# Optimization experiments

Hardware: AMD Instinct MI355X
Metric: run time of the kernel (lower is better)

Reference implementation:

```python
import jax, jax.numpy as jnp
from jax import lax
import numpy as np

B, N, CF = 16, 4096, 64
NPOINT, NSAMPLE = 1024, 32
MLP = (64, 64, 128)
IN_CH = CF + 3
EPS = 1e-5


def _fps(xyz, npoint):
    # Farthest point sampling; deterministic start at index 0 (original uses a random start).
    Bn = xyz.shape[0]
    d0 = jnp.full(xyz.shape[:2], 1e10, xyz.dtype)
    f0 = jnp.zeros((Bn,), jnp.int32)
    def step(carry, _):
        dist, far = carry
        c = jnp.take_along_axis(xyz, far[:, None, None], axis=1)  # (B,1,3)
        d = jnp.sum((xyz - c) ** 2, axis=-1)                      # (B,N)
        dist = jnp.minimum(dist, d)
        return (dist, jnp.argmax(dist, axis=1).astype(jnp.int32)), far
    _, idxs = lax.scan(step, (d0, f0), None, length=npoint)
    return jnp.transpose(idxs)  # (B, npoint)


def _gather(pts, idx):
    # pts (B,N,C), idx (B,...) int -> (B,...,C)
    return jax.vmap(lambda p, i: p[i])(pts, idx)


def _bn_relu(x, g, b, axes):
    # training-mode batch norm (batch statistics), channel axis = 1
    m = jnp.mean(x, axes, keepdims=True)
    v = jnp.var(x, axes, keepdims=True)
    sh = (1, -1) + (1,) * (x.ndim - 2)
    return jax.nn.relu((x - m) * lax.rsqrt(v + EPS) * g.reshape(sh) + b.reshape(sh))


def _forward(xyz, points, density, params):
    fps_idx = _fps(xyz, NPOINT)
    new_xyz = _gather(xyz, fps_idx)  # (B,S,3)
    # source query_ball_point sorts distances and keeps the nsample nearest -> kNN
    d = (jnp.sum(new_xyz ** 2, -1)[:, :, None] + jnp.sum(xyz ** 2, -1)[:, None, :]
         - 2.0 * jnp.einsum('bsc,bnc->bsn', new_xyz, xyz))  # (B,S,N)
    _, idx = lax.top_k(-d, NSAMPLE)  # (B,S,ns) nearest neighbors
    gxyz = _gather(xyz, idx) - new_xyz[:, :, None, :]           # (B,S,ns,3)
    gpts = _gather(jnp.transpose(points, (0, 2, 1)), idx)       # (B,S,ns,CF)
    x = jnp.transpose(jnp.concatenate([gxyz, gpts], -1), (0, 3, 1, 2))  # (B,IN_CH,S,ns)
    (w0, b0, g0, be0, w1, b1, g1, be1, w2, b2, g2, be2, wd, bd, gd, bed) = params
    for w, b, g, be in ((w0, b0, g0, be0), (w1, b1, g1, be1), (w2, b2, g2, be2)):
        x = _bn_relu(jnp.einsum('oc,bcsk->bosk', w, x) + b[None, :, None, None], g, be, (0, 2, 3))
    # density weighting at sampled centers
    dcen = jnp.transpose(_gather(jnp.transpose(density, (0, 2, 1)), fps_idx), (0, 2, 1))  # (B,1,S)
    dw = _bn_relu(jnp.einsum('oc,bcs->bos', wd, dcen) + bd[None, :, None], gd, bed, (0, 2))  # (B,Cout,S)
    x = x * dw[..., None]
    return new_xyz, jnp.max(x, axis=-1)  # (B,S,3), (B,Cout,S)


def setup_inputs() -> dict:
    key = jax.random.key(0)
    ks = jax.random.split(key, 3)
    inp = {
        'xyz': jax.random.normal(ks[0], (B, N, 3), jnp.float32),
        'points': jax.random.normal(ks[1], (B, CF, N), jnp.float32),
        'density': jax.random.uniform(ks[2], (B, 1, N), jnp.float32),
    }
    chans = (IN_CH,) + MLP
    for i in range(3):
        cin, cout = chans[i], chans[i + 1]
        inp[f'w{i}'] = jax.random.normal(jax.random.fold_in(key, 10 + i), (cout, cin), jnp.float32) / np.sqrt(cin).astype(np.float32)
        inp[f'b{i}'] = jnp.zeros((cout,), jnp.float32)
        inp[f'g{i}'] = jnp.ones((cout,), jnp.float32)
        inp[f'be{i}'] = jnp.zeros((cout,), jnp.float32)
    inp['wd'] = jax.random.normal(jax.random.fold_in(key, 20), (MLP[-1], 1), jnp.float32)
    inp['bd'] = jnp.zeros((MLP[-1],), jnp.float32)
    inp['gd'] = jnp.ones((MLP[-1],), jnp.float32)
    inp['bed'] = jnp.zeros((MLP[-1],), jnp.float32)
    return inp


def reference(xyz, points, density, w0, b0, g0, be0, w1, b1, g1, be1, w2, b2, g2, be2, wd, bd, gd, bed):
    return _forward(xyz, points, density,
                    (w0, b0, g0, be0, w1, b1, g1, be1, w2, b2, g2, be2, wd, bd, gd, bed))
```

## Files before the change

### kernel.cpp

```cpp
#include <hip/hip_runtime.h>
#include <hip/hip_bf16.h>
#include <stdint.h>

#define NB 16
#define NN 4096
#define NCF 64
#define NS 1024
#define NK 32
#define NPTS (NB*NS*NK)
#define CIN 67
#define EPSV 1e-5f

static __device__ __forceinline__ float fmul(float a, float b){ return __fmul_rn(a,b); }
static __device__ __forceinline__ float fadd(float a, float b){ return __fadd_rn(a,b); }
static __device__ __forceinline__ float fsub(float a, float b){ return __fsub_rn(a,b); }

typedef float f2 __attribute__((ext_vector_type(2)));
#define PK_ADD(d,a,b) asm("v_pk_add_f32 %0, %1, %2" : "=v"(d) : "v"(a), "v"(b))
#define PK_MUL(d,a,b) asm("v_pk_mul_f32 %0, %1, %2" : "=v"(d) : "v"(a), "v"(b))

static __device__ __forceinline__ unsigned short f2b(float f){
  unsigned u = __float_as_uint(f);
  return (unsigned short)((u + 0x7FFFu + ((u>>16)&1u)) >> 16);
}

template<int CTRL>
static __device__ __forceinline__ float dppmax_f32(float x){
  float o = __uint_as_float((unsigned)__builtin_amdgcn_update_dpp(
      0, (int)__float_as_uint(x), CTRL, 0xf, 0xf, true));
  return fmaxf(x, o);
}
static __device__ __forceinline__ float wave_max63_f32(float x){
  x = dppmax_f32<0x111>(x);
  x = dppmax_f32<0x112>(x);
  x = dppmax_f32<0x114>(x);
  x = dppmax_f32<0x118>(x);
  x = dppmax_f32<0x142>(x);
  x = dppmax_f32<0x143>(x);
  return x;
}
template<int CTRL>
static __device__ __forceinline__ float dppadd_f32(float x){
  float o = __uint_as_float((unsigned)__builtin_amdgcn_update_dpp(
      0, (int)__float_as_uint(x), CTRL, 0xf, 0xf, true));
  return x + o;
}
static __device__ __forceinline__ float wave_sum63_f32(float x){
  x = dppadd_f32<0x111>(x);
  x = dppadd_f32<0x112>(x);
  x = dppadd_f32<0x114>(x);
  x = dppadd_f32<0x118>(x);
  x = dppadd_f32<0x142>(x);
  x = dppadd_f32<0x143>(x);
  return x;
}
static __device__ __forceinline__ float half_sum31_f32(float x){
  x = dppadd_f32<0x111>(x);
  x = dppadd_f32<0x112>(x);
  x = dppadd_f32<0x114>(x);
  x = dppadd_f32<0x118>(x);
  x = dppadd_f32<0x142>(x);
  return x;
}
static __device__ __forceinline__ float group8_max_f32(float x){
  x = dppmax_f32<0xB1>(x);
  x = dppmax_f32<0x4E>(x);
  x = dppmax_f32<0x141>(x);
  return x;
}
static __device__ __forceinline__ unsigned long long readlane_u64(unsigned long long v, int l){
  unsigned lo = (unsigned)__builtin_amdgcn_readlane((int)(unsigned)v, l);
  unsigned hi = (unsigned)__builtin_amdgcn_readlane((int)(unsigned)(v>>32), l);
  return ((unsigned long long)hi<<32) | lo;
}
static __device__ __forceinline__ unsigned long long wave_shr1_u64(unsigned long long x){
  unsigned lo = (unsigned)__builtin_amdgcn_update_dpp(
      0, (int)(unsigned)x, 0x138, 0xf, 0xf, true);
  unsigned hi = (unsigned)__builtin_amdgcn_update_dpp(
      0, (int)(unsigned)(x>>32), 0x138, 0xf, 0xf, true);
  return ((unsigned long long)hi<<32) | lo;
}

__global__ __launch_bounds__(256) void prep_kernel(const float* __restrict__ pts,
    const float* __restrict__ xyz, float* __restrict__ ptsT, float* __restrict__ sqx){
  int blk = blockIdx.x;
  int b = blk >> 4;
  int n = ((blk & 15) << 8) + threadIdx.x;
  const float* src = pts + (size_t)b*NCF*NN + n;
  float v[NCF];
  #pragma unroll
  for (int c=0;c<NCF;c++) v[c] = src[(size_t)c*NN];
  float4* dst = (float4*)(ptsT + ((size_t)b*NN + n)*NCF);
  #pragma unroll
  for (int j=0;j<16;j++) dst[j] = make_float4(v[4*j],v[4*j+1],v[4*j+2],v[4*j+3]);
  const float* xp = xyz + ((size_t)b*NN + n)*3;
  float x=xp[0], y=xp[1], z=xp[2];
  sqx[(size_t)b*NN+n] = fadd(fadd(fmul(x,x),fmul(y,y)),fmul(z,z));
}

#define FT 256
__global__ __launch_bounds__(FT) void fps_kernel(const float* __restrict__ xyz,
    int* __restrict__ fidx, float* __restrict__ newxyz){
  int b = blockIdx.x;
  __shared__ float4 s4[NN];
  __shared__ unsigned long long candK[2][4];
  __shared__ float4 candC[2][4];
  const int tid = threadIdx.x;
  const int lane = tid & 63;
  const int wv = tid >> 6;
  for (int i = tid; i < NN; i += FT){
    const float* p = xyz + ((size_t)b*NN + i)*3;
    s4[i] = make_float4(p[0], p[1], p[2], 0.f);
  }
  __syncthreads();
  f2 px[8], py[8], pz[8], d2[8];
  #pragma unroll
  for (int m=0;m<8;m++){
    float4 a = s4[tid*16 + 2*m];
    float4 c = s4[tid*16 + 2*m + 1];
    px[m] = (f2){a.x, c.x};
    py[m] = (f2){a.y, c.y};
    pz[m] = (f2){a.z, c.z};
    d2[m] = (f2){1e10f, 1e10f};
  }
  int far = 0;
  float4 cc = s4[0];
  for (int s=0;s<NS;s++){
    if (tid==0){
      fidx[b*NS+s] = far;
      float* o = newxyz + ((size_t)b*NS+s)*3;
      o[0]=cc.x; o[1]=cc.y; o[2]=cc.z;
    }
    f2 ncx = (f2){-cc.x,-cc.x}, ncy = (f2){-cc.y,-cc.y}, ncz = (f2){-cc.z,-cc.z};
    float bv = -1.0f; int bj = 0;
    #pragma unroll
    for (int m=0;m<8;m++){
      f2 dx,dy,dz,xx,yy,zz,ss,dd;
      PK_ADD(dx, px[m], ncx);
      PK_ADD(dy, py[m], ncy);
      PK_ADD(dz, pz[m], ncz);
      PK_MUL(xx, dx, dx);
      PK_MUL(yy, dy, dy);
      PK_ADD(ss, xx, yy);
      PK_MUL(zz, dz, dz);
      PK_ADD(dd, ss, zz);
      float u0 = fminf(d2[m].x, dd.x);
      float u1 = fminf(d2[m].y, dd.y);
      d2[m].x = u0; d2[m].y = u1;
      if (u0 > bv){ bv = u0; bj = 2*m; }
      if (u1 > bv){ bv = u1; bj = 2*m+1; }
    }
    int nbest = (tid<<4) + bj;
    float mv = wave_max63_f32(bv);
    float mvu = __uint_as_float((unsigned)__builtin_amdgcn_readlane(
        (int)__float_as_uint(mv), 63));
    unsigned long long tiedm = __ballot(bv == mvu);
    int wl = __ffsll(tiedm) - 1;
    unsigned nwin = (unsigned)__builtin_amdgcn_readlane(nbest, wl);
    if (lane == wl){
      float4 cw = s4[nwin];
      candK[s&1][wv] = ((unsigned long long)__float_as_uint(mvu) << 32)
                     | (unsigned long long)(unsigned)~nwin;
      candC[s&1][wv] = cw;
    }
    __syncthreads();
    const ulonglong2* kp = (const ulonglong2*)candK[s&1];
    ulonglong2 k01v = kp[0], k23v = kp[1];
    float4 C0 = candC[s&1][0], C1 = candC[s&1][1];
    float4 C2 = candC[s&1][2], C3 = candC[s&1][3];
    bool a01 = k01v.y > k01v.x;
    unsigned long long k01 = a01 ? k01v.y : k01v.x;
    float4 c01; c01.x = a01?C1.x:C0.x; c01.y = a01?C1.y:C0.y; c01.z = a01?C1.z:C0.z;
    bool a23 = k23v.y > k23v.x;
    unsigned long long k23 = a23 ? k23v.y : k23v.x;
    float4 c23; c23.x = a23?C3.x:C2.x; c23.y = a23?C3.y:C2.y; c23.z = a23?C3.z:C2.z;
    bool af = k23 > k01;
    unsigned long long kk = af ? k23 : k01;
    cc.x = af?c23.x:c01.x; cc.y = af?c23.y:c01.y; cc.z = af?c23.z:c01.z;
    far = (int)(~(unsigned)kk) & (NN-1);
  }
}

__global__ __launch_bounds__(256) void dcen_kernel(const float* __restrict__ density,
    const int* __restrict__ fidx, float* __restrict__ dcen){
  int i = blockIdx.x*256 + threadIdx.x;
  int b = i >> 10;
  dcen[i] = density[(size_t)b*NN + fidx[i]];
}

__global__ __launch_bounds__(256) void dstats_kernel(const float* __restrict__ dcen,
    float* __restrict__ dstat){
  float s=0.f, q=0.f;
  for (int i=threadIdx.x; i<NB*NS; i+=256){ float v=dcen[i]; s+=v; q+=v*v; }
  __shared__ float ls[256], lq[256];
  ls[threadIdx.x]=s; lq[threadIdx.x]=q;
  __syncthreads();
  for (int off=128; off>0; off>>=1){
    if (threadIdx.x<off){ ls[threadIdx.x]+=ls[threadIdx.x+off]; lq[threadIdx.x]+=lq[threadIdx.x+off]; }
    __syncthreads();
  }
  if (threadIdx.x==0){
    float m = ls[0]/(float)(NB*NS);
    dstat[0]=m; dstat[1]=lq[0]/(float)(NB*NS) - m*m;
  }
}

__global__ __launch_bounds__(256) void knn_kernel(const float* __restrict__ xyz,
    const float* __restrict__ sqx, const float* __restrict__ newxyz,
    int* __restrict__ kidx){
  const int lane = threadIdx.x & 63;
  const int g = blockIdx.x*4 + (threadIdx.x >> 6);
  const int b = g >> 10;
  const float* cp = newxyz + (size_t)g*3;
  const float cx=cp[0], cy=cp[1], cz=cp[2];
  const float sqc = fadd(fadd(fmul(cx,cx),fmul(cy,cy)),fmul(cz,cz));
  const float* xb  = xyz + (size_t)b*NN*3;
  const float* sqb = sqx + (size_t)b*NN;
  unsigned long long kept  = ~0ULL;
  unsigned long long worst = ~0ULL;
  for (int n0=0; n0<NN; n0+=64){
    const int n = n0 + lane;
    const float* xp = xb + (size_t)n*3;
    float x=xp[0], y=xp[1], z=xp[2];
    float dot = fadd(fadd(fmul(cx,x),fmul(cy,y)),fmul(cz,z));
    float d = fsub(fadd(sqc, sqb[n]), fmul(2.0f,dot));
    unsigned u = __float_as_uint(d);
    u = (u & 0x80000000u) ? ~u : (u | 0x80000000u);
    unsigned long long ck = ((unsigned long long)u << 32) | (unsigned)n;
    unsigned long long mask = __ballot(ck < worst);
    while (mask){
      const int l = __ffsll(mask) - 1;
      mask &= mask - 1;
      const unsigned long long k = readlane_u64(ck, l);
      if (k < worst){
        bool m = kept > k;
        unsigned long long M = __ballot(m) << 1;
        unsigned long long sh = wave_shr1_u64(kept);
        bool msh = (M >> lane) & 1ULL;
        unsigned long long ins = msh ? sh : k;
        kept = m ? ins : kept;
        worst = readlane_u64(kept, 31);
      }
    }
  }
  if (lane < 32) kidx[(size_t)g*NK + lane] = (int)(kept & 0xFFFFFFFFULL);
}

__global__ __launch_bounds__(256) void conv1_kernel(const float* __restrict__ xyz,
    const float* __restrict__ ptsT, const float* __restrict__ newxyz,
    const int* __restrict__ kidx, const float* __restrict__ w0,
    const float* __restrict__ b0, unsigned short* __restrict__ z1,
    float* __restrict__ partial){
  __shared__ float si[CIN][128];
  __shared__ float sw[CIN][64];
  __shared__ float sbias[64];
  const int tid = threadIdx.x;
  for (int i = tid; i < CIN*64; i += 256){
    int o = i / CIN, c = i - o*CIN;
    sw[c][o] = w0[i];
  }
  if (tid < 64) sbias[tid] = b0[tid];
  const int p0 = blockIdx.x * 128;
  if (tid < 128){
    const int p = p0 + tid;
    const int g = p >> 5;
    const int b = g >> 10;
    const int n = kidx[p];
    const float* xp = xyz + ((size_t)b*NN + n)*3;
    const float* cp = newxyz + (size_t)g*3;
    si[0][tid] = xp[0]-cp[0];
    si[1][tid] = xp[1]-cp[1];
    si[2][tid] = xp[2]-cp[2];
    const float4* pr = (const float4*)(ptsT + ((size_t)b*NN + n)*NCF);
    #pragma unroll
    for (int j=0;j<16;j++){
      float4 v = pr[j];
      si[3+4*j][tid]=v.x; si[4+4*j][tid]=v.y; si[5+4*j][tid]=v.z; si[6+4*j][tid]=v.w;
    }
  }
  __syncthreads();
  const int og = tid >> 6;
  const int pg = tid & 63;
  float acc0[16], acc1[16];
  #pragma unroll
  for (int j=0;j<16;j++){ float bv = sbias[og*16+j]; acc0[j]=bv; acc1[j]=bv; }
  for (int c=0;c<CIN;c++){
    float2 a = *(const float2*)&si[c][2*pg];
    const float4* wr = (const float4*)&sw[c][og*16];
    #pragma unroll
    for (int q=0;q<4;q++){
      float4 w = wr[q];
      acc0[4*q+0]+=a.x*w.x; acc0[4*q+1]+=a.x*w.y; acc0[4*q+2]+=a.x*w.z; acc0[4*q+3]+=a.x*w.w;
      acc1[4*q+0]+=a.y*w.x; acc1[4*q+1]+=a.y*w.y; acc1[4*q+2]+=a.y*w.z; acc1[4*q+3]+=a.y*w.w;
    }
  }
  unsigned v[8];
  #pragma unroll
  for (int j=0;j<8;j++) v[j] = (unsigned)f2b(acc0[2*j]) | ((unsigned)f2b(acc0[2*j+1])<<16);
  uint4* d0 = (uint4*)(z1 + (size_t)(p0+2*pg)*64 + og*16);
  d0[0]=make_uint4(v[0],v[1],v[2],v[3]); d0[1]=make_uint4(v[4],v[5],v[6],v[7]);
  #pragma unroll
  for (int j=0;j<8;j++) v[j] = (unsigned)f2b(acc1[2*j]) | ((unsigned)f2b(acc1[2*j+1])<<16);
  uint4* d1 = (uint4*)(z1 + (size_t)(p0+2*pg+1)*64 + og*16);
  d1[0]=make_uint4(v[0],v[1],v[2],v[3]); d1[1]=make_uint4(v[4],v[5],v[6],v[7]);
  #pragma unroll
  for (int j=0;j<16;j++){
    float s = wave_sum63_f32(acc0[j]+acc1[j]);
    float q = wave_sum63_f32(acc0[j]*acc0[j] + acc1[j]*acc1[j]);
    if (pg==63){
      partial[(size_t)blockIdx.x*128 + og*16 + j] = s;
      partial[(size_t)blockIdx.x*128 + 64 + og*16 + j] = q;
    }
  }
}

__global__ __launch_bounds__(256) void conv2_kernel(const unsigned short* __restrict__ z1,
    const float* __restrict__ w1, const float* __restrict__ b1,
    const float* __restrict__ scale1, const float* __restrict__ shift1,
    unsigned short* __restrict__ z2, float* __restrict__ partial){
  __shared__ float si[64][128];
  __shared__ float sw[64][64];
  __shared__ float sbias[64];
  const int tid = threadIdx.x;
  for (int i = tid; i < 64*64; i += 256){
    int o = i >> 6, c = i & 63;
    sw[c][o] = w1[i];
  }
  if (tid < 64) sbias[tid] = b1[tid];
  const int p0 = blockIdx.x * 128;
  if (tid < 128){
    const uint4* zr = (const uint4*)(z1 + (size_t)(p0 + tid)*64);
    #pragma unroll
    for (int j=0;j<8;j++){
      uint4 vv = zr[j];
      unsigned a[4] = {vv.x, vv.y, vv.z, vv.w};
      #pragma unroll
      for (int t=0;t<4;t++){
        int c = j*8 + t*2;
        float lo = __uint_as_float(a[t] << 16);
        float hi = __uint_as_float(a[t] & 0xFFFF0000u);
        si[c][tid]   = fmaxf(lo*scale1[c]   + shift1[c],   0.0f);
        si[c+1][tid] = fmaxf(hi*scale1[c+1] + shift1[c+1], 0.0f);
      }
    }
  }
  __syncthreads();
  const int og = tid >> 6;
  const int pg = tid & 63;
  float acc0[16], acc1[16];
  #pragma unroll
  for (int j=0;j<16;j++){ float bv = sbias[og*16+j]; acc0[j]=bv; acc1[j]=bv; }
  for (int c=0;c<64;c++){
    float2 a = *(const float2*)&si[c][2*pg];
    const float4* wr = (const float4*)&sw[c][og*16];
    #pragma unroll
    for (int q=0;q<4;q++){
      float4 w = wr[q];
      acc0[4*q+0]+=a.x*w.x; acc0[4*q+1]+=a.x*w.y; acc0[4*q+2]+=a.x*w.z; acc0[4*q+3]+=a.x*w.w;
      acc1[4*q+0]+=a.y*w.x; acc1[4*q+1]+=a.y*w.y; acc1[4*q+2]+=a.y*w.z; acc1[4*q+3]+=a.y*w.w;
    }
  }
  unsigned v[8];
  #pragma unroll
  for (int j=0;j<8;j++) v[j] = (unsigned)f2b(acc0[2*j]) | ((unsigned)f2b(acc0[2*j+1])<<16);
  uint4* d0 = (uint4*)(z2 + (size_t)(p0+2*pg)*64 + og*16);
  d0[0]=make_uint4(v[0],v[1],v[2],v[3]); d0[1]=make_uint4(v[4],v[5],v[6],v[7]);
  #pragma unroll
  for (int j=0;j<8;j++) v[j] = (unsigned)f2b(acc1[2*j]) | ((unsigned)f2b(acc1[2*j+1])<<16);
  uint4* d1 = (uint4*)(z2 + (size_t)(p0+2*pg+1)*64 + og*16);
  d1[0]=make_uint4(v[0],v[1],v[2],v[3]); d1[1]=make_uint4(v[4],v[5],v[6],v[7]);
  #pragma unroll
  for (int j=0;j<16;j++){
    float s = wave_sum63_f32(acc0[j]+acc1[j]);
    float q = wave_sum63_f32(acc0[j]*acc0[j] + acc1[j]*acc1[j]);
    if (pg==63){
      partial[(size_t)blockIdx.x*128 + og*16 + j] = s;
      partial[(size_t)blockIdx.x*128 + 64 + og*16 + j] = q;
    }
  }
}

__global__ __launch_bounds__(256) void conv3_kernel(const unsigned short* __restrict__ z2,
    const float* __restrict__ w2, const float* __restrict__ b2,
    const float* __restrict__ scale2, const float* __restrict__ shift2,
    float* __restrict__ m3, float* __restrict__ partial){
  __shared__ float si[64][128];
  __shared__ float sw[64][128];
  const int tid = threadIdx.x;
  for (int i = tid; i < 64*128; i += 256){
    int o = i >> 6, c = i & 63;
    sw[c][o] = w2[i];
  }
  const int p0 = blockIdx.x * 128;
  if (tid < 128){
    const uint4* zr = (const uint4*)(z2 + (size_t)(p0 + tid)*64);
    #pragma unroll
    for (int j=0;j<8;j++){
      uint4 vv = zr[j];
      unsigned a[4]={vv.x,vv.y,vv.z,vv.w};
      #pragma unroll
      for (int t=0;t<4;t++){
        int c = j*8+t*2;
        float lo=__uint_as_float(a[t]<<16), hi=__uint_as_float(a[t]&0xFFFF0000u);
        si[c][tid]   = fmaxf(lo*scale2[c]+shift2[c],0.f);
        si[c+1][tid] = fmaxf(hi*scale2[c+1]+shift2[c+1],0.f);
      }
    }
  }
  __syncthreads();
  const int og = tid >> 5;
  const int pg = tid & 31;
  float acc[4][16];
  const float4* bq = (const float4*)(b2 + og*16);
  #pragma unroll
  for (int q=0;q<4;q++){
    float4 bb = bq[q];
    #pragma unroll
    for (int p=0;p<4;p++){ acc[p][4*q]=bb.x; acc[p][4*q+1]=bb.y; acc[p][4*q+2]=bb.z; acc[p][4*q+3]=bb.w; }
  }
  for (int c=0;c<64;c++){
    float4 a = *(const float4*)&si[c][pg*4];
    const float4* wr = (const float4*)&sw[c][og*16];
    float ap[4] = {a.x, a.y, a.z, a.w};
    #pragma unroll
    for (int q=0;q<4;q++){
      float4 w = wr[q];
      #pragma unroll
      for (int p=0;p<4;p++){
        acc[p][4*q+0]+=ap[p]*w.x; acc[p][4*q+1]+=ap[p]*w.y;
        acc[p][4*q+2]+=ap[p]*w.z; acc[p][4*q+3]+=ap[p]*w.w;
      }
    }
  }
  float mx[16];
  #pragma unroll
  for (int j=0;j<16;j++){
    float m = fmaxf(fmaxf(acc[0][j],acc[1][j]), fmaxf(acc[2][j],acc[3][j]));
    mx[j] = group8_max_f32(m);
  }
  if ((pg & 7)==0){
    const int center = blockIdx.x*4 + (pg>>3);
    float4* mp = (float4*)(m3 + (size_t)center*128 + og*16);
    #pragma unroll
    for (int q=0;q<4;q++) mp[q] = make_float4(mx[4*q],mx[4*q+1],mx[4*q+2],mx[4*q+3]);
  }
  #pragma unroll
  for (int j=0;j<16;j++){
    float s = half_sum31_f32(acc[0][j]+acc[1][j]+acc[2][j]+acc[3][j]);
    float q = half_sum31_f32(acc[0][j]*acc[0][j]+acc[1][j]*acc[1][j]
                            +acc[2][j]*acc[2][j]+acc[3][j]*acc[3][j]);
    if (pg==31){
      partial[(size_t)blockIdx.x*256 + og*16 + j] = s;
      partial[(size_t)blockIdx.x*256 + 128 + og*16 + j] = q;
    }
  }
}

__global__ __launch_bounds__(256) void mkbn_kernel(const float* __restrict__ partial,
    int nrows, int stride, const float* __restrict__ g, const float* __restrict__ be,
    float* __restrict__ scale, float* __restrict__ shift, float inv_count){
  const int c = blockIdx.x;
  const int C = gridDim.x;
  float s=0.f, q=0.f;
  for (int r=threadIdx.x; r<nrows; r+=256){
    s += partial[(size_t)r*stride + c];
    q += partial[(size_t)r*stride + C + c];
  }
  __shared__ float ls[256], lq[256];
  ls[threadIdx.x]=s; lq[threadIdx.x]=q;
  __syncthreads();
  for (int off=128; off>0; off>>=1){
    if (threadIdx.x < off){ ls[threadIdx.x]+=ls[threadIdx.x+off]; lq[threadIdx.x]+=lq[threadIdx.x+off]; }
    __syncthreads();
  }
  if (threadIdx.x==0){
    float mean = ls[0]*inv_count;
    float var  = lq[0]*inv_count - mean*mean;
    float sc = g[c]*rsqrtf(var + EPSV);
    scale[c]=sc; shift[c]=be[c]-mean*sc;
  }
}

__global__ __launch_bounds__(256) void final_kernel(const float* __restrict__ m3,
    const float* __restrict__ dcen, const float* __restrict__ scale3,
    const float* __restrict__ shift3, const float* __restrict__ wd,
    const float* __restrict__ bd, const float* __restrict__ gd,
    const float* __restrict__ bed, const float* __restrict__ dstat,
    float* __restrict__ out){
  size_t i = (size_t)blockIdx.x*256 + threadIdx.x;
  int s  = (int)(i & 1023);
  int ch = (int)((i >> 10) & 127);
  int b  = (int)(i >> 17);
  float mean_d = dstat[0], var_d = dstat[1];
  float w = wd[ch];
  float meanp = w*mean_d + bd[ch];
  float varp  = w*w*var_d;
  float dsc = gd[ch]*rsqrtf(varp + EPSV);
  float dsh = bed[ch] - meanp*dsc;
  float pre = w*dcen[b*NS+s] + bd[ch];
  float dw  = fmaxf(dsc*pre + dsh, 0.0f);
  float z   = m3[((size_t)(b*NS+s))*128 + ch];
  float x   = fmaxf(scale3[ch]*z + shift3[ch], 0.0f);
  out[i] = x*dw;
}

extern "C" void kernel_launch(void* const* d_in, const int* in_sizes, int n_in,
                              void* d_out, int out_size, void* d_ws, size_t ws_size,
                              hipStream_t stream){
  const float* xyz     = (const float*)d_in[0];
  const float* points  = (const float*)d_in[1];
  const float* density = (const float*)d_in[2];
  const float* w0 = (const float*)d_in[3];
  const float* b0 = (const float*)d_in[4];
  const float* g0 = (const float*)d_in[5];
  const float* be0= (const float*)d_in[6];
  const float* w1 = (const float*)d_in[7];
  const float* b1 = (const float*)d_in[8];
  const float* g1 = (const float*)d_in[9];
  const float* be1= (const float*)d_in[10];
  const float* w2 = (const float*)d_in[11];
  const float* b2 = (const float*)d_in[12];
  const float* g2 = (const float*)d_in[13];
  const float* be2= (const float*)d_in[14];
  const float* wd = (const float*)d_in[15];
  const float* bd = (const float*)d_in[16];
  const float* gd = (const float*)d_in[17];
  const float* bed= (const float*)d_in[18];

  float* out = (float*)d_out;
  float* newxyz = out;
  float* out1   = out + (size_t)NB*NS*3;

  float* ptsT = (float*)d_ws;
  float* sqx  = ptsT + (size_t)NB*NN*NCF;
  int*   fidx = (int*)(sqx + (size_t)NB*NN);
  float* dcen = (float*)(fidx + NB*NS);
  int*   kidx = (int*)(dcen + NB*NS);
  unsigned short* z1 = (unsigned short*)(kidx + NPTS);
  unsigned short* z2 = z1 + (size_t)NPTS*64;
  float* m3   = (float*)(z2 + (size_t)NPTS*64);
  float* p1   = m3 + (size_t)NB*NS*128;
  float* p2   = p1 + 4096*128;
  float* p3   = p2 + 4096*128;
  float* bnp  = p3 + 4096*256;
  float* dstat= bnp + 512;

  hipLaunchKernelGGL(prep_kernel,  dim3(256),  dim3(256), 0, stream, points, xyz, ptsT, sqx);
  hipLaunchKernelGGL(fps_kernel,   dim3(NB),   dim3(FT),  0, stream, xyz, fidx, newxyz);
  hipLaunchKernelGGL(dcen_kernel,  dim3(64),   dim3(256), 0, stream, density, fidx, dcen);
  hipLaunchKernelGGL(dstats_kernel,dim3(1),    dim3(256), 0, stream, dcen, dstat);
  hipLaunchKernelGGL(knn_kernel,   dim3(4096), dim3(256), 0, stream, xyz, sqx, newxyz, kidx);
  hipLaunchKernelGGL(conv1_kernel, dim3(4096), dim3(256), 0, stream, xyz, ptsT, newxyz, kidx, w0, b0, z1, p1);
  hipLaunchKernelGGL(mkbn_kernel,  dim3(64),   dim3(256), 0, stream, p1, 4096, 128, g0, be0, bnp+0,   bnp+64,  1.0f/(float)NPTS);
  hipLaunchKernelGGL(conv2_kernel, dim3(4096), dim3(256), 0, stream, z1, w1, b1, bnp+0, bnp+64, z2, p2);
  hipLaunchKernelGGL(mkbn_kernel,  dim3(64),   dim3(256), 0, stream, p2, 4096, 128, g1, be1, bnp+128, bnp+192, 1.0f/(float)NPTS);
  hipLaunchKernelGGL(conv3_kernel, dim3(4096), dim3(256), 0, stream, z2, w2, b2, bnp+128, bnp+192, m3, p3);
  hipLaunchKernelGGL(mkbn_kernel,  dim3(128),  dim3(256), 0, stream, p3, 4096, 256, g2, be2, bnp+256, bnp+384, 1.0f/(float)NPTS);
  hipLaunchKernelGGL(final_kernel, dim3(8192), dim3(256), 0, stream, m3, dcen, bnp+256, bnp+384, wd, bd, gd, bed, dstat, out1);
}
```

Before: 1.331 ms.

## Widen FPS to 512 threads and use packed FP32 FMA in conv kernels

The FPS kernel now runs 512 threads per batch with 8 points per thread. The cross-wave reduction is simplified: each wave publishes only its packed distance/index key, and the winner's coordinates are read from shared memory after the max. The conv1, conv2 and conv3 inner loops switch from scalar FMAs to v_pk_fma_f32 on float2 accumulators, and the batch-norm statistic reductions are packed the same way. This aims to cut per-iteration FPS latency and halve FMA issue count in the convolutions, at the cost of an extra dependent LDS read per FPS step and more inline-asm register pressure.

```diff
diff --git a/kernel.cpp b/kernel.cpp
--- a/kernel.cpp
+++ b/kernel.cpp
@@ -18,10 +18,18 @@
 typedef float f2 __attribute__((ext_vector_type(2)));
 #define PK_ADD(d,a,b) asm("v_pk_add_f32 %0, %1, %2" : "=v"(d) : "v"(a), "v"(b))
 #define PK_MUL(d,a,b) asm("v_pk_mul_f32 %0, %1, %2" : "=v"(d) : "v"(a), "v"(b))
+#define PK_FMA(d,a,b) asm("v_pk_fma_f32 %0, %1, %2, %0" : "+v"(d) : "v"(a), "v"(b))
+static __device__ __forceinline__ f2 pk_add(f2 a, f2 b){ f2 d; PK_ADD(d,a,b); return d; }
+static __device__ __forceinline__ f2 pk_mul(f2 a, f2 b){ f2 d; PK_MUL(d,a,b); return d; }
 
 static __device__ __forceinline__ unsigned short f2b(float f){
   unsigned u = __float_as_uint(f);
   return (unsigned short)((u + 0x7FFFu + ((u>>16)&1u)) >> 16);
+}
+
+static __device__ __forceinline__ unsigned long long umax64(unsigned long long a,
+                                                            unsigned long long b){
+  return a > b ? a : b;
 }
 
 template<int CTRL>
@@ -39,33 +47,36 @@
   x = dppmax_f32<0x143>(x);
   return x;
 }
-template<int CTRL>
-static __device__ __forceinline__ float dppadd_f32(float x){
-  float o = __uint_as_float((unsigned)__builtin_amdgcn_update_dpp(
-      0, (int)__float_as_uint(x), CTRL, 0xf, 0xf, true));
-  return x + o;
-}
-static __device__ __forceinline__ float wave_sum63_f32(float x){
-  x = dppadd_f32<0x111>(x);
-  x = dppadd_f32<0x112>(x);
-  x = dppadd_f32<0x114>(x);
-  x = dppadd_f32<0x118>(x);
-  x = dppadd_f32<0x142>(x);
-  x = dppadd_f32<0x143>(x);
-  return x;
-}
-static __device__ __forceinline__ float half_sum31_f32(float x){
-  x = dppadd_f32<0x111>(x);
-  x = dppadd_f32<0x112>(x);
-  x = dppadd_f32<0x114>(x);
-  x = dppadd_f32<0x118>(x);
-  x = dppadd_f32<0x142>(x);
-  return x;
-}
 static __device__ __forceinline__ float group8_max_f32(float x){
   x = dppmax_f32<0xB1>(x);
   x = dppmax_f32<0x4E>(x);
   x = dppmax_f32<0x141>(x);
+  return x;
+}
+template<int CTRL>
+static __device__ __forceinline__ f2 dppadd_f2(f2 x){
+  f2 o;
+  o.x = __uint_as_float((unsigned)__builtin_amdgcn_update_dpp(
+      0, (int)__float_as_uint(x.x), CTRL, 0xf, 0xf, true));
+  o.y = __uint_as_float((unsigned)__builtin_amdgcn_update_dpp(
+      0, (int)__float_as_uint(x.y), CTRL, 0xf, 0xf, true));
+  return pk_add(x, o);
+}
+static __device__ __forceinline__ f2 wave_sum63_f2(f2 x){
+  x = dppadd_f2<0x111>(x);
+  x = dppadd_f2<0x112>(x);
+  x = dppadd_f2<0x114>(x);
+  x = dppadd_f2<0x118>(x);
+  x = dppadd_f2<0x142>(x);
+  x = dppadd_f2<0x143>(x);
+  return x;
+}
+static __device__ __forceinline__ f2 half_sum31_f2(f2 x){
+  x = dppadd_f2<0x111>(x);
+  x = dppadd_f2<0x112>(x);
+  x = dppadd_f2<0x114>(x);
+  x = dppadd_f2<0x118>(x);
+  x = dppadd_f2<0x142>(x);
   return x;
 }
 static __device__ __forceinline__ unsigned long long readlane_u64(unsigned long long v, int l){
@@ -98,13 +109,12 @@
   sqx[(size_t)b*NN+n] = fadd(fadd(fmul(x,x),fmul(y,y)),fmul(z,z));
 }
 
-#define FT 256
+#define FT 512
 __global__ __launch_bounds__(FT) void fps_kernel(const float* __restrict__ xyz,
     int* __restrict__ fidx, float* __restrict__ newxyz){
   int b = blockIdx.x;
   __shared__ float4 s4[NN];
-  __shared__ unsigned long long candK[2][4];
-  __shared__ float4 candC[2][4];
+  __shared__ unsigned long long candK[2][8];
   const int tid = threadIdx.x;
   const int lane = tid & 63;
   const int wv = tid >> 6;
@@ -113,11 +123,11 @@
     s4[i] = make_float4(p[0], p[1], p[2], 0.f);
   }
   __syncthreads();
-  f2 px[8], py[8], pz[8], d2[8];
-  #pragma unroll
-  for (int m=0;m<8;m++){
-    float4 a = s4[tid*16 + 2*m];
-    float4 c = s4[tid*16 + 2*m + 1];
+  f2 px[4], py[4], pz[4], d2[4];
+  #pragma unroll
+  for (int m=0;m<4;m++){
+    float4 a = s4[tid*8 + 2*m];
+    float4 c = s4[tid*8 + 2*m + 1];
     px[m] = (f2){a.x, c.x};
     py[m] = (f2){a.y, c.y};
     pz[m] = (f2){a.z, c.z};
@@ -134,7 +144,7 @@
     f2 ncx = (f2){-cc.x,-cc.x}, ncy = (f2){-cc.y,-cc.y}, ncz = (f2){-cc.z,-cc.z};
     float bv = -1.0f; int bj = 0;
     #pragma unroll
-    for (int m=0;m<8;m++){
+    for (int m=0;m<4;m++){
       f2 dx,dy,dz,xx,yy,zz,ss,dd;
       PK_ADD(dx, px[m], ncx);
       PK_ADD(dy, py[m], ncy);
@@ -150,34 +160,24 @@
       if (u0 > bv){ bv = u0; bj = 2*m; }
       if (u1 > bv){ bv = u1; bj = 2*m+1; }
     }
-    int nbest = (tid<<4) + bj;
+    int nbest = (tid<<3) + bj;
     float mv = wave_max63_f32(bv);
     float mvu = __uint_as_float((unsigned)__builtin_amdgcn_readlane(
         (int)__float_as_uint(mv), 63));
     unsigned long long tiedm = __ballot(bv == mvu);
     int wl = __ffsll(tiedm) - 1;
     unsigned nwin = (unsigned)__builtin_amdgcn_readlane(nbest, wl);
-    if (lane == wl){
-      float4 cw = s4[nwin];
+    if (lane == 0)
       candK[s&1][wv] = ((unsigned long long)__float_as_uint(mvu) << 32)
                      | (unsigned long long)(unsigned)~nwin;
-      candC[s&1][wv] = cw;
-    }
     __syncthreads();
-    const ulonglong2* kp = (const ulonglong2*)candK[s&1];
-    ulonglong2 k01v = kp[0], k23v = kp[1];
-    float4 C0 = candC[s&1][0], C1 = candC[s&1][1];
-    float4 C2 = candC[s&1][2], C3 = candC[s&1][3];
-    bool a01 = k01v.y > k01v.x;
-    unsigned long long k01 = a01 ? k01v.y : k01v.x;
-    float4 c01; c01.x = a01?C1.x:C0.x; c01.y = a01?C1.y:C0.y; c01.z = a01?C1.z:C0.z;
-    bool a23 = k23v.y > k23v.x;
-    unsigned long long k23 = a23 ? k23v.y : k23v.x;
-    float4 c23; c23.x = a23?C3.x:C2.x; c23.y = a23?C3.y:C2.y; c23.z = a23?C3.z:C2.z;
-    bool af = k23 > k01;
-    unsigned long long kk = af ? k23 : k01;
-    cc.x = af?c23.x:c01.x; cc.y = af?c23.y:c01.y; cc.z = af?c23.z:c01.z;
+    const ulonglong2* cp = (const ulonglong2*)candK[s&1];
+    ulonglong2 c0=cp[0], c1=cp[1], c2=cp[2], c3=cp[3];
+    unsigned long long kk = umax64(
+        umax64(umax64(c0.x,c0.y), umax64(c1.x,c1.y)),
+        umax64(umax64(c2.x,c2.y), umax64(c3.x,c3.y)));
     far = (int)(~(unsigned)kk) & (NN-1);
+    cc = s4[far];
   }
 }
 
@@ -281,35 +281,41 @@
   __syncthreads();
   const int og = tid >> 6;
   const int pg = tid & 63;
-  float acc0[16], acc1[16];
-  #pragma unroll
-  for (int j=0;j<16;j++){ float bv = sbias[og*16+j]; acc0[j]=bv; acc1[j]=bv; }
+  f2 acc0[8], acc1[8];
+  const f2* bp = (const f2*)&sbias[og*16];
+  #pragma unroll
+  for (int q=0;q<8;q++){ f2 bb = bp[q]; acc0[q]=bb; acc1[q]=bb; }
   for (int c=0;c<CIN;c++){
     float2 a = *(const float2*)&si[c][2*pg];
-    const float4* wr = (const float4*)&sw[c][og*16];
-    #pragma unroll
-    for (int q=0;q<4;q++){
-      float4 w = wr[q];
-      acc0[4*q+0]+=a.x*w.x; acc0[4*q+1]+=a.x*w.y; acc0[4*q+2]+=a.x*w.z; acc0[4*q+3]+=a.x*w.w;
-      acc1[4*q+0]+=a.y*w.x; acc1[4*q+1]+=a.y*w.y; acc1[4*q+2]+=a.y*w.z; acc1[4*q+3]+=a.y*w.w;
+    const f2* wr = (const f2*)&sw[c][og*16];
+    f2 a0 = (f2){a.x, a.x};
+    f2 a1 = (f2){a.y, a.y};
+    #pragma unroll
+    for (int q=0;q<8;q++){
+      f2 w = wr[q];
+      PK_FMA(acc0[q], a0, w);
+      PK_FMA(acc1[q], a1, w);
     }
   }
   unsigned v[8];
   #pragma unroll
-  for (int j=0;j<8;j++) v[j] = (unsigned)f2b(acc0[2*j]) | ((unsigned)f2b(acc0[2*j+1])<<16);
+  for (int j=0;j<8;j++) v[j] = (unsigned)f2b(acc0[j].x) | ((unsigned)f2b(acc0[j].y)<<16);
   uint4* d0 = (uint4*)(z1 + (size_t)(p0+2*pg)*64 + og*16);
   d0[0]=make_uint4(v[0],v[1],v[2],v[3]); d0[1]=make_uint4(v[4],v[5],v[6],v[7]);
   #pragma unroll
-  for (int j=0;j<8;j++) v[j] = (unsigned)f2b(acc1[2*j]) | ((unsigned)f2b(acc1[2*j+1])<<16);
+  for (int j=0;j<8;j++) v[j] = (unsigned)f2b(acc1[j].x) | ((unsigned)f2b(acc1[j].y)<<16);
   uint4* d1 = (uint4*)(z1 + (size_t)(p0+2*pg+1)*64 + og*16);
   d1[0]=make_uint4(v[0],v[1],v[2],v[3]); d1[1]=make_uint4(v[4],v[5],v[6],v[7]);
   #pragma unroll
-  for (int j=0;j<16;j++){
-    float s = wave_sum63_f32(acc0[j]+acc1[j]);
-    float q = wave_sum63_f32(acc0[j]*acc0[j] + acc1[j]*acc1[j]);
+  for (int q=0;q<8;q++){
+    f2 s = pk_add(acc0[q], acc1[q]);
+    f2 sq = pk_add(pk_mul(acc0[q],acc0[q]), pk_mul(acc1[q],acc1[q]));
+    s = wave_sum63_f2(s);
+    sq = wave_sum63_f2(sq);
     if (pg==63){
-      partial[(size_t)blockIdx.x*128 + og*16 + j] = s;
-      partial[(size_t)blockIdx.x*128 + 64 + og*16 + j] = q;
+      float* pb = partial + (size_t)blockIdx.x*128 + og*16;
+      pb[2*q]=s.x; pb[2*q+1]=s.y;
+      pb[64+2*q]=sq.x; pb[64+2*q+1]=sq.y;
     }
   }
 }
@@ -347,35 +353,41 @@
   __syncthreads();
   const int og = tid >> 6;
   const int pg = tid & 63;
-  float acc0[16], acc1[16];
-  #pragma unroll
-  for (int j=0;j<16;j++){ float bv = sbias[og*16+j]; acc0[j]=bv; acc1[j]=bv; }
+  f2 acc0[8], acc1[8];
+  const f2* bp = (const f2*)&sbias[og*16];
+  #pragma unroll
+  for (int q=0;q<8;q++){ f2 bb = bp[q]; acc0[q]=bb; acc1[q]=bb; }
   for (int c=0;c<64;c++){
     float2 a = *(const float2*)&si[c][2*pg];
-    const float4* wr = (const float4*)&sw[c][og*16];
-    #pragma unroll
-    for (int q=0;q<4;q++){
-      float4 w = wr[q];
-      acc0[4*q+0]+=a.x*w.x; acc0[4*q+1]+=a.x*w.y; acc0[4*q+2]+=a.x*w.z; acc0[4*q+3]+=a.x*w.w;
-      acc1[4*q+0]+=a.y*w.x; acc1[4*q+1]+=a.y*w.y; acc1[4*q+2]+=a.y*w.z; acc1[4*q+3]+=a.y*w.w;
+    const f2* wr = (const f2*)&sw[c][og*16];
+    f2 a0 = (f2){a.x, a.x};
+    f2 a1 = (f2){a.y, a.y};
+    #pragma unroll
+    for (int q=0;q<8;q++){
+      f2 w = wr[q];
+      PK_FMA(acc0[q], a0, w);
+      PK_FMA(acc1[q], a1, w);
     }
   }
   unsigned v[8];
   #pragma unroll
-  for (int j=0;j<8;j++) v[j] = (unsigned)f2b(acc0[2*j]) | ((unsigned)f2b(acc0[2*j+1])<<16);
+  for (int j=0;j<8;j++) v[j] = (unsigned)f2b(acc0[j].x) | ((unsigned)f2b(acc0[j].y)<<16);
   uint4* d0 = (uint4*)(z2 + (size_t)(p0+2*pg)*64 + og*16);
   d0[0]=make_uint4(v[0],v[1],v[2],v[3]); d0[1]=make_uint4(v[4],v[5],v[6],v[7]);
   #pragma unroll
-  for (int j=0;j<8;j++) v[j] = (unsigned)f2b(acc1[2*j]) | ((unsigned)f2b(acc1[2*j+1])<<16);
+  for (int j=0;j<8;j++) v[j] = (unsigned)f2b(acc1[j].x) | ((unsigned)f2b(acc1[j].y)<<16);
   uint4* d1 = (uint4*)(z2 + (size_t)(p0+2*pg+1)*64 + og*16);
   d1[0]=make_uint4(v[0],v[1],v[2],v[3]); d1[1]=make_uint4(v[4],v[5],v[6],v[7]);
   #pragma unroll
-  for (int j=0;j<16;j++){
-    float s = wave_sum63_f32(acc0[j]+acc1[j]);
-    float q = wave_sum63_f32(acc0[j]*acc0[j] + acc1[j]*acc1[j]);
+  for (int q=0;q<8;q++){
+    f2 s = pk_add(acc0[q], acc1[q]);
+    f2 sq = pk_add(pk_mul(acc0[q],acc0[q]), pk_mul(acc1[q],acc1[q]));
+    s = wave_sum63_f2(s);
+    sq = wave_sum63_f2(sq);
     if (pg==63){
-      partial[(size_t)blockIdx.x*128 + og*16 + j] = s;
-      partial[(size_t)blockIdx.x*128 + 64 + og*16 + j] = q;
+      float* pb = partial + (size_t)blockIdx.x*128 + og*16;
+      pb[2*q]=s.x; pb[2*q+1]=s.y;
+      pb[64+2*q]=sq.x; pb[64+2*q+1]=sq.y;
     }
   }
 }
@@ -410,33 +422,34 @@
   __syncthreads();
   const int og = tid >> 5;
   const int pg = tid & 31;
-  float acc[4][16];
-  const float4* bq = (const float4*)(b2 + og*16);
-  #pragma unroll
-  for (int q=0;q<4;q++){
-    float4 bb = bq[q];
-    #pragma unroll
-    for (int p=0;p<4;p++){ acc[p][4*q]=bb.x; acc[p][4*q+1]=bb.y; acc[p][4*q+2]=bb.z; acc[p][4*q+3]=bb.w; }
+  f2 acc[4][8];
+  const f2* bq = (const f2*)(b2 + og*16);
+  #pragma unroll
+  for (int q=0;q<8;q++){
+    f2 bb = bq[q];
+    #pragma unroll
+    for (int p=0;p<4;p++) acc[p][q]=bb;
   }
   for (int c=0;c<64;c++){
     float4 a = *(const float4*)&si[c][pg*4];
-    const float4* wr = (const float4*)&sw[c][og*16];
-    float ap[4] = {a.x, a.y, a.z, a.w};
-    #pragma unroll
-    for (int q=0;q<4;q++){
-      float4 w = wr[q];
-      #pragma unroll
-      for (int p=0;p<4;p++){
-        acc[p][4*q+0]+=ap[p]*w.x; acc[p][4*q+1]+=ap[p]*w.y;
-        acc[p][4*q+2]+=ap[p]*w.z; acc[p][4*q+3]+=ap[p]*w.w;
-      }
+    const f2* wr = (const f2*)&sw[c][og*16];
+    f2 a0=(f2){a.x,a.x}, a1=(f2){a.y,a.y}, a2=(f2){a.z,a.z}, a3=(f2){a.w,a.w};
+    #pragma unroll
+    for (int q=0;q<8;q++){
+      f2 w = wr[q];
+      PK_FMA(acc[0][q], a0, w);
+      PK_FMA(acc[1][q], a1, w);
+      PK_FMA(acc[2][q], a2, w);
+      PK_FMA(acc[3][q], a3, w);
     }
   }
   float mx[16];
   #pragma unroll
-  for (int j=0;j<16;j++){
-    float m = fmaxf(fmaxf(acc[0][j],acc[1][j]), fmaxf(acc[2][j],acc[3][j]));
-    mx[j] = group8_max_f32(m);
+  for (int q=0;q<8;q++){
+    float mxx = fmaxf(fmaxf(acc[0][q].x,acc[1][q].x), fmaxf(acc[2][q].x,acc[3][q].x));
+    float mxy = fmaxf(fmaxf(acc[0][q].y,acc[1][q].y), fmaxf(acc[2][q].y,acc[3][q].y));
+    mx[2*q]   = group8_max_f32(mxx);
+    mx[2*q+1] = group8_max_f32(mxy);
   }
   if ((pg & 7)==0){
     const int center = blockIdx.x*4 + (pg>>3);
@@ -445,13 +458,16 @@
     for (int q=0;q<4;q++) mp[q] = make_float4(mx[4*q],mx[4*q+1],mx[4*q+2],mx[4*q+3]);
   }
   #pragma unroll
-  for (int j=0;j<16;j++){
-    float s = half_sum31_f32(acc[0][j]+acc[1][j]+acc[2][j]+acc[3][j]);
-    float q = half_sum31_f32(acc[0][j]*acc[0][j]+acc[1][j]*acc[1][j]
-                            +acc[2][j]*acc[2][j]+acc[3][j]*acc[3][j]);
+  for (int q=0;q<8;q++){
+    f2 s = pk_add(pk_add(acc[0][q],acc[1][q]), pk_add(acc[2][q],acc[3][q]));
+    f2 sq = pk_add(pk_add(pk_mul(acc[0][q],acc[0][q]), pk_mul(acc[1][q],acc[1][q])),
+                   pk_add(pk_mul(acc[2][q],acc[2][q]), pk_mul(acc[3][q],acc[3][q])));
+    s = half_sum31_f2(s);
+    sq = half_sum31_f2(sq);
     if (pg==31){
-      partial[(size_t)blockIdx.x*256 + og*16 + j] = s;
-      partial[(size_t)blockIdx.x*256 + 128 + og*16 + j] = q;
+      float* pb = partial + (size_t)blockIdx.x*256 + og*16;
+      pb[2*q]=s.x; pb[2*q+1]=s.y;
+      pb[128+2*q]=sq.x; pb[128+2*q+1]=sq.y;
     }
   }
 }
```

Result: no change. 1.345 ms (+1.0%).
